# Kernel tuning notes

Measured on AMD Instinct MI355X. Metric: run time of the kernel, lower is better.

The kernel has to match this reference:

```python
import jax, jax.numpy as jnp
import numpy as np

B, T, D, H = 4, 2048, 1024, 16
DH = D // H  # 64


def setup_inputs() -> dict:
    key = jax.random.key(0)
    ks = jax.random.split(key, 6)
    s = 0.02
    x = jax.random.normal(ks[0], (B, T, D), dtype=jnp.float32)
    # causal mask: True (1) marks positions to be masked out
    mask = jnp.triu(jnp.ones((T, T), dtype=bool), k=1)[None, None, :, :]
    WQ = jax.random.normal(ks[1], (D, D), dtype=jnp.float32) * s
    WK = jax.random.normal(ks[2], (D, D), dtype=jnp.float32) * s
    WV = jax.random.normal(ks[3], (D, D), dtype=jnp.float32) * s
    WO = jax.random.normal(ks[4], (D, D), dtype=jnp.float32) * s
    z = jnp.zeros((D,), dtype=jnp.float32)
    return {"x": x, "mask": mask, "WQ": WQ, "bQ": z, "WK": WK, "bK": z,
            "WV": WV, "bV": z, "WO": WO, "bO": z}


def reference(x, mask, WQ, bQ, WK, bK, WV, bV, WO, bO):
    Bc, Tc, Dc = x.shape
    def split_heads(t):  # [B,T,D] -> [B,H,T,DH]
        return t.reshape(Bc, Tc, H, DH).transpose(0, 2, 1, 3)
    q = split_heads(x @ WQ + bQ)
    k = split_heads(x @ WK + bK)
    v = split_heads(x @ WV + bV)
    qk = jnp.einsum("bhqd,bhkd->bhqk", q, k) / jnp.sqrt(jnp.float32(DH))
    qk = qk + mask.astype(qk.dtype) * (-1e9)
    attn = jax.nn.softmax(qk, axis=-1)
    ctx = jnp.einsum("bhqk,bhkd->bhqd", attn, v)  # [B,H,T,DH]
    ctx = ctx.transpose(0, 2, 1, 3).reshape(Bc, Tc, Dc)
    return ctx @ WO + bO
```

## Files before the change

### kernel.cpp

```cpp
#include <hip/hip_runtime.h>
#include <hip/hip_bf16.h>
#include <stdint.h>

#define T_SEQ   2048
#define D_MODEL 1024
#define NHEAD   16
#define DHEAD   64
#define BATCH   4
#define MTOK    (BATCH * T_SEQ)

typedef __attribute__((ext_vector_type(4))) float f32x4;
typedef __attribute__((ext_vector_type(16))) float f32x16;
typedef __attribute__((ext_vector_type(8))) short bf16x8;
typedef __attribute__((ext_vector_type(4))) short s16x4;
typedef __attribute__((ext_vector_type(4))) unsigned u32x4;

__device__ __forceinline__ f32x4 mfma16(bf16x8 a, bf16x8 b, f32x4 c) {
  return __builtin_amdgcn_mfma_f32_16x16x32_bf16(a, b, c, 0, 0, 0);
}
__device__ __forceinline__ f32x16 mfma32(bf16x8 a, bf16x8 b, f32x16 c) {
  return __builtin_amdgcn_mfma_f32_32x32x16_bf16(a, b, c, 0, 0, 0);
}

__device__ __forceinline__ short f2bf(float f) {
  __hip_bfloat16 h = __float2bfloat16(f);
  return *reinterpret_cast<short*>(&h);
}

__device__ __forceinline__ unsigned cvtpk(float a, float b) {
  unsigned r;
  asm("v_cvt_pk_bf16_f32 %0, %1, %2" : "=v"(r) : "v"(a), "v"(b));
  return r;
}

union PB { u32x4 u; bf16x8 b; };

#define GLD_LDS16(gp, lp)                                                      \
  __builtin_amdgcn_global_load_lds(                                            \
      (const __attribute__((address_space(1))) void*)(gp),                     \
      (__attribute__((address_space(3))) void*)(lp), 16, 0, 0)

__global__ __launch_bounds__(256) void transpose_w_kernel(
    const float* __restrict__ W0, const float* __restrict__ W1,
    const float* __restrict__ W2, const float* __restrict__ W3,
    short* __restrict__ out)
{
  const int z = blockIdx.z;
  const float* W = (z == 0) ? W0 : (z == 1) ? W1 : (z == 2) ? W2 : W3;
  short* o = out + (size_t)z * D_MODEL * D_MODEL;
  __shared__ float tile[32][33];
  const int n0 = blockIdx.x * 32, k0 = blockIdx.y * 32;
  const int c = threadIdx.x & 31, r = threadIdx.x >> 5;
#pragma unroll
  for (int i = 0; i < 4; i++)
    tile[r + i * 8][c] = W[(size_t)(k0 + r + i * 8) * D_MODEL + n0 + c];
  __syncthreads();
#pragma unroll
  for (int i = 0; i < 4; i++)
    o[(size_t)(n0 + r + i * 8) * D_MODEL + k0 + c] = f2bf(tile[c][r + i * 8]);
}

__global__ __launch_bounds__(256) void cvt_x_kernel(
    const float* __restrict__ x, short* __restrict__ xb)
{
  const size_t i = (size_t)blockIdx.x * 256 + threadIdx.x;
  const float4 a = ((const float4*)x)[i * 2];
  const float4 b = ((const float4*)x)[i * 2 + 1];
  bf16x8 o;
  o[0] = f2bf(a.x); o[1] = f2bf(a.y); o[2] = f2bf(a.z); o[3] = f2bf(a.w);
  o[4] = f2bf(b.x); o[5] = f2bf(b.y); o[6] = f2bf(b.z); o[7] = f2bf(b.w);
  ((bf16x8*)xb)[i] = o;
}

__global__ __launch_bounds__(256) void gemm_bt(
    const short* __restrict__ A, const short* __restrict__ Bt,
    const float* __restrict__ bias, float* __restrict__ Cp)
{
  __shared__ __align__(16) short As[128 * 32];
  __shared__ __align__(16) short Bs[128 * 32];
  const int tid = threadIdx.x, lane = tid & 63, wid = tid >> 6;
  const int wr = wid >> 1, wc = wid & 1;
  const int lg = lane >> 4, ln = lane & 15;
  const int m0 = blockIdx.x * 128, n0 = blockIdx.y * 128;
  const int lrow = lane >> 2, lchunk = lane & 3;

  f32x4 acc[4][4];
#pragma unroll
  for (int i = 0; i < 4; i++)
#pragma unroll
    for (int j = 0; j < 4; j++) acc[i][j] = {0.f, 0.f, 0.f, 0.f};

  for (int k0 = 0; k0 < 1024; k0 += 32) {
#pragma unroll
    for (int s = 0; s < 2; ++s) {
      const int rbase = (wid * 2 + s) * 16;
      const short* gpa = A + (size_t)(m0 + rbase + lrow) * 1024 + k0 + lchunk * 8;
      GLD_LDS16(gpa, As + rbase * 32);
      const short* gpb = Bt + (size_t)(n0 + rbase + lrow) * 1024 + k0 + lchunk * 8;
      GLD_LDS16(gpb, Bs + rbase * 32);
    }
    __syncthreads();
    bf16x8 a[4], b[4];
#pragma unroll
    for (int mi = 0; mi < 4; mi++)
      a[mi] = *(const bf16x8*)(As + (wr * 64 + mi * 16 + ln) * 32 + lg * 8);
#pragma unroll
    for (int ni = 0; ni < 4; ni++)
      b[ni] = *(const bf16x8*)(Bs + (wc * 64 + ni * 16 + ln) * 32 + lg * 8);
#pragma unroll
    for (int mi = 0; mi < 4; mi++)
#pragma unroll
      for (int ni = 0; ni < 4; ni++)
        acc[mi][ni] = mfma16(a[mi], b[ni], acc[mi][ni]);
    __syncthreads();
  }

#pragma unroll
  for (int mi = 0; mi < 4; mi++)
#pragma unroll
    for (int ni = 0; ni < 4; ni++)
#pragma unroll
      for (int r = 0; r < 4; r++) {
        const int row = m0 + wr * 64 + mi * 16 + lg * 4 + r;
        const int col = n0 + wc * 64 + ni * 16 + ln;
        Cp[(size_t)row * 1024 + col] = acc[mi][ni][r] + bias[col];
      }
}

__global__ __launch_bounds__(256) void gemm_qkv(
    const short* __restrict__ A, const short* __restrict__ Wt,
    const float* __restrict__ bQ, const float* __restrict__ bK,
    const float* __restrict__ bV,
    short* __restrict__ Qb, short* __restrict__ Kb, short* __restrict__ Vb,
    float qscale)
{
  __shared__ __align__(16) short As[128 * 32];
  __shared__ __align__(16) short Bs[128 * 32];
  const int tid = threadIdx.x, lane = tid & 63, wid = tid >> 6;
  const int wr = wid >> 1, wc = wid & 1;
  const int lg = lane >> 4, ln = lane & 15;
  const int m0 = blockIdx.x * 128;
  const int nglob = blockIdx.y * 128;
  const int seg = blockIdx.y >> 3;
  const int n0 = nglob & 1023;
  const short* Bt = Wt + (size_t)nglob * 1024;
  const float* bias = (seg == 0) ? bQ : (seg == 1) ? bK : bV;
  short* Cp = (seg == 0) ? Qb : (seg == 1) ? Kb : Vb;
  const float scale = (seg == 0) ? qscale : 1.0f;
  const int lrow = lane >> 2, lchunk = lane & 3;

  f32x4 acc[4][4];
#pragma unroll
  for (int i = 0; i < 4; i++)
#pragma unroll
    for (int j = 0; j < 4; j++) acc[i][j] = {0.f, 0.f, 0.f, 0.f};

  for (int k0 = 0; k0 < 1024; k0 += 32) {
#pragma unroll
    for (int s = 0; s < 2; ++s) {
      const int rbase = (wid * 2 + s) * 16;
      const short* gpa = A + (size_t)(m0 + rbase + lrow) * 1024 + k0 + lchunk * 8;
      GLD_LDS16(gpa, As + rbase * 32);
      const short* gpb = Bt + (size_t)(rbase + lrow) * 1024 + k0 + lchunk * 8;
      GLD_LDS16(gpb, Bs + rbase * 32);
    }
    __syncthreads();
    bf16x8 a[4], b[4];
#pragma unroll
    for (int mi = 0; mi < 4; mi++)
      a[mi] = *(const bf16x8*)(As + (wr * 64 + mi * 16 + ln) * 32 + lg * 8);
#pragma unroll
    for (int ni = 0; ni < 4; ni++)
      b[ni] = *(const bf16x8*)(Bs + (wc * 64 + ni * 16 + ln) * 32 + lg * 8);
#pragma unroll
    for (int mi = 0; mi < 4; mi++)
#pragma unroll
      for (int ni = 0; ni < 4; ni++)
        acc[mi][ni] = mfma16(a[mi], b[ni], acc[mi][ni]);
    __syncthreads();
  }

#pragma unroll
  for (int mi = 0; mi < 4; mi++)
#pragma unroll
    for (int ni = 0; ni < 4; ni++)
#pragma unroll
      for (int r = 0; r < 4; r++) {
        const int row = m0 + wr * 64 + mi * 16 + lg * 4 + r;
        const int col = n0 + wc * 64 + ni * 16 + ln;
        const float v = (acc[mi][ni][r] + bias[col]) * scale;
        Cp[(size_t)row * 1024 + col] = f2bf(v);
      }
}

__global__ __launch_bounds__(256) void transpose_v_kernel(
    const short* __restrict__ V, short* __restrict__ Vt)
{
  const int bh = blockIdx.y, t0 = blockIdx.x * 64;
  const int b = bh >> 4, h = bh & 15;
  __shared__ __align__(16) short tile[64][72];
  const int tl = threadIdx.x >> 3, c = threadIdx.x & 7;
#pragma unroll
  for (int half = 0; half < 2; half++) {
    const int t = tl + half * 32;
    bf16x8 v = *(const bf16x8*)(V + (size_t)(b * T_SEQ + t0 + t) * 1024 + h * 64 + c * 8);
    *(bf16x8*)&tile[t][c * 8] = v;
  }
  __syncthreads();
#pragma unroll
  for (int half = 0; half < 2; half++) {
    const int dh = tl + half * 32;
    bf16x8 v;
#pragma unroll
    for (int j = 0; j < 8; j++) v[j] = tile[c * 8 + j][dh];
    *(bf16x8*)(Vt + ((size_t)bh * 64 + dh) * T_SEQ + t0 + c * 8) = v;
  }
}

__device__ __forceinline__ void tile_chain(
    const bf16x8* kf0, const bf16x8* kf1,
    const bf16x8* vf0, const bf16x8* vf1,
    const bf16x8* qf,
    f32x16& o0, f32x16& o1, float& m_run, float& l_run,
    const int kv0, const int qw, const int q, const int hi)
{
  f32x16 s0, s1;
#pragma unroll
  for (int i = 0; i < 16; i++) { s0[i] = 0.f; s1[i] = 0.f; }
  __builtin_amdgcn_s_setprio(1);
#pragma unroll
  for (int c = 0; c < 4; c++) s0 = mfma32(kf0[c], qf[c], s0);
#pragma unroll
  for (int c = 0; c < 4; c++) s1 = mfma32(kf1[c], qf[c], s1);
  __builtin_amdgcn_s_setprio(0);

  if (kv0 + 63 > qw) {
    const int qrel = q - kv0 - 4 * hi;
#pragma unroll
    for (int r = 0; r < 16; r++) {
      const int cst = (r & 3) + 8 * (r >> 2);
      if (cst > qrel) s0[r] = -3.0e38f;
      if (cst + 32 > qrel) s1[r] = -3.0e38f;
    }
  }

  float mx;
  {
    float t[8];
#pragma unroll
    for (int i = 0; i < 8; i++)
      t[i] = fmaxf(fmaxf(s0[i], s0[i + 8]), fmaxf(s1[i], s1[i + 8]));
    const float a0 = fmaxf(fmaxf(t[0], t[1]), fmaxf(t[2], t[3]));
    const float a1 = fmaxf(fmaxf(t[4], t[5]), fmaxf(t[6], t[7]));
    mx = fmaxf(a0, a1);
    mx = fmaxf(mx, __shfl_xor(mx, 32));
  }
  const float mn = fmaxf(m_run, mx);
  const float rr = exp2f(m_run - mn);
  m_run = mn;
#pragma unroll
  for (int i = 0; i < 16; i++) s0[i] = exp2f(s0[i] - mn);
#pragma unroll
  for (int i = 0; i < 16; i++) s1[i] = exp2f(s1[i] - mn);
  float ts;
  {
    float t[8];
#pragma unroll
    for (int i = 0; i < 8; i++) t[i] = (s0[i] + s0[i + 8]) + (s1[i] + s1[i + 8]);
    ts = ((t[0] + t[1]) + (t[2] + t[3])) + ((t[4] + t[5]) + (t[6] + t[7]));
    ts += __shfl_xor(ts, 32);
  }
  l_run = l_run * rr + ts;
#pragma unroll
  for (int i = 0; i < 16; i++) { o0[i] *= rr; o1[i] *= rr; }

  const bool low = (hi == 0);
  PB pb[4];
  {
    unsigned c0 = cvtpk(s0[0], s0[1]),   c1 = cvtpk(s0[2], s0[3]);
    unsigned c2 = cvtpk(s0[4], s0[5]),   c3 = cvtpk(s0[6], s0[7]);
    unsigned c4 = cvtpk(s0[8], s0[9]),   c5 = cvtpk(s0[10], s0[11]);
    unsigned c6 = cvtpk(s0[12], s0[13]), c7 = cvtpk(s0[14], s0[15]);
    unsigned d0 = __shfl_xor((int)c0, 32), d1 = __shfl_xor((int)c1, 32);
    unsigned d2 = __shfl_xor((int)c2, 32), d3 = __shfl_xor((int)c3, 32);
    unsigned d4 = __shfl_xor((int)c4, 32), d5 = __shfl_xor((int)c5, 32);
    unsigned d6 = __shfl_xor((int)c6, 32), d7 = __shfl_xor((int)c7, 32);
    pb[0].u = (u32x4){low ? c0 : d2, low ? c1 : d3, low ? d0 : c2, low ? d1 : c3};
    pb[1].u = (u32x4){low ? c4 : d6, low ? c5 : d7, low ? d4 : c6, low ? d5 : c7};
  }
  {
    unsigned c0 = cvtpk(s1[0], s1[1]),   c1 = cvtpk(s1[2], s1[3]);
    unsigned c2 = cvtpk(s1[4], s1[5]),   c3 = cvtpk(s1[6], s1[7]);
    unsigned c4 = cvtpk(s1[8], s1[9]),   c5 = cvtpk(s1[10], s1[11]);
    unsigned c6 = cvtpk(s1[12], s1[13]), c7 = cvtpk(s1[14], s1[15]);
    unsigned d0 = __shfl_xor((int)c0, 32), d1 = __shfl_xor((int)c1, 32);
    unsigned d2 = __shfl_xor((int)c2, 32), d3 = __shfl_xor((int)c3, 32);
    unsigned d4 = __shfl_xor((int)c4, 32), d5 = __shfl_xor((int)c5, 32);
    unsigned d6 = __shfl_xor((int)c6, 32), d7 = __shfl_xor((int)c7, 32);
    pb[2].u = (u32x4){low ? c0 : d2, low ? c1 : d3, low ? d0 : c2, low ? d1 : c3};
    pb[3].u = (u32x4){low ? c4 : d6, low ? c5 : d7, low ? d4 : c6, low ? d5 : c7};
  }

  __builtin_amdgcn_s_setprio(1);
#pragma unroll
  for (int kc = 0; kc < 4; kc++) {
    o0 = mfma32(vf0[kc], pb[kc].b, o0);
    o1 = mfma32(vf1[kc], pb[kc].b, o1);
  }
  __builtin_amdgcn_s_setprio(0);
}

__device__ __forceinline__ void attn_epilogue(
    short* cp, const f32x16& o0, const f32x16& o1, float l_run, int hi)
{
  const float inv = 1.0f / l_run;
#pragma unroll
  for (int g = 0; g < 4; g++) {
    s16x4 w0, w1;
#pragma unroll
    for (int j = 0; j < 4; j++) {
      w0[j] = f2bf(o0[g * 4 + j] * inv);
      w1[j] = f2bf(o1[g * 4 + j] * inv);
    }
    *(s16x4*)(cp + g * 8 + 4 * hi) = w0;
    *(s16x4*)(cp + 32 + g * 8 + 4 * hi) = w1;
  }
}

#define LOADK(dst0, dst1, itv)                                                 \
  {                                                                            \
    const short* kp = K + (size_t)(b * T_SEQ + (itv) * 64 + lq) * 1024 +       \
                      h * 64 + hi * 8;                                         \
    _Pragma("unroll")                                                          \
    for (int c = 0; c < 4; c++) {                                              \
      dst0[c] = *(const bf16x8*)(kp + c * 16);                                 \
      dst1[c] = *(const bf16x8*)(kp + 32 * 1024 + c * 16);                     \
    }                                                                          \
  }

#define LOADV(dst0, dst1, itv)                                                 \
  {                                                                            \
    const short* vp = Vt + (size_t)(bh * 64 + lq) * T_SEQ + (itv) * 64 +       \
                      hi * 8;                                                  \
    _Pragma("unroll")                                                          \
    for (int c = 0; c < 4; c++) {                                              \
      dst0[c] = *(const bf16x8*)(vp + c * 16);                                 \
      dst1[c] = *(const bf16x8*)(vp + 32 * T_SEQ + c * 16);                    \
    }                                                                          \
  }

__global__ __launch_bounds__(256, 2) void attn_fwd(
    const short* __restrict__ Q, const short* __restrict__ K,
    const short* __restrict__ Vt, short* __restrict__ ctx)
{
  const int tid = threadIdx.x, lane = tid & 63, wid = tid >> 6;
  const int hi = lane >> 5, lq = lane & 31;
  const int id = (int)blockIdx.x;
  const int bh = (id & 7) * 8 + ((id >> 3) & 7);
  const int p = (id >> 6) * 4 + wid;
  const int b = bh >> 4, h = bh & 15;

  const int qtA = p, qtB = 63 - p;
  const int qwA = qtA * 32, qwB = qtB * 32;
  const int qA = qwA + lq, qB = qwB + lq;

  bf16x8 qfA[4], qfB[4];
  {
    const short* qpA = Q + (size_t)(b * T_SEQ + qA) * 1024 + h * 64 + hi * 8;
    const short* qpB = Q + (size_t)(b * T_SEQ + qB) * 1024 + h * 64 + hi * 8;
#pragma unroll
    for (int c = 0; c < 4; c++) {
      qfA[c] = *(const bf16x8*)(qpA + c * 16);
      qfB[c] = *(const bf16x8*)(qpB + c * 16);
    }
  }

  f32x16 oA0, oA1, oB0, oB1;
#pragma unroll
  for (int i = 0; i < 16; i++) { oA0[i] = 0.f; oA1[i] = 0.f; oB0[i] = 0.f; oB1[i] = 0.f; }
  float mA = -3.0e38f, lA = 0.f, mB = -3.0e38f, lB = 0.f;

  const int ntA = (qwA + 95) >> 6, ntB = (qwB + 95) >> 6;

  bf16x8 kP0[4], kP1[4], kQ0[4], kQ1[4];
  LOADK(kP0, kP1, 0);

  int it = 0;
#pragma unroll 1
  for (; it + 2 <= ntB; it += 2) {
    {
      bf16x8 vf0[4], vf1[4];
      LOADV(vf0, vf1, it);
      LOADK(kQ0, kQ1, it + 1);
      tile_chain(kP0, kP1, vf0, vf1, qfB, oB0, oB1, mB, lB, it * 64, qwB, qB, hi);
      if (it < ntA)
        tile_chain(kP0, kP1, vf0, vf1, qfA, oA0, oA1, mA, lA, it * 64, qwA, qA, hi);
    }
    {
      bf16x8 vf0[4], vf1[4];
      LOADV(vf0, vf1, it + 1);
      if (it + 2 < ntB) LOADK(kP0, kP1, it + 2);
      tile_chain(kQ0, kQ1, vf0, vf1, qfB, oB0, oB1, mB, lB, (it + 1) * 64, qwB, qB, hi);
      if (it + 1 < ntA)
        tile_chain(kQ0, kQ1, vf0, vf1, qfA, oA0, oA1, mA, lA, (it + 1) * 64, qwA, qA, hi);
    }
  }
  if (it < ntB) {
    bf16x8 vf0[4], vf1[4];
    LOADV(vf0, vf1, it);
    tile_chain(kP0, kP1, vf0, vf1, qfB, oB0, oB1, mB, lB, it * 64, qwB, qB, hi);
    if (it < ntA)
      tile_chain(kP0, kP1, vf0, vf1, qfA, oA0, oA1, mA, lA, it * 64, qwA, qA, hi);
  }

  attn_epilogue(ctx + (size_t)(b * T_SEQ + qA) * 1024 + h * 64, oA0, oA1, lA, hi);
  attn_epilogue(ctx + (size_t)(b * T_SEQ + qB) * 1024 + h * 64, oB0, oB1, lB, hi);
}

extern "C" void kernel_launch(void* const* d_in, const int* in_sizes, int n_in,
                              void* d_out, int out_size, void* d_ws, size_t ws_size,
                              hipStream_t stream)
{
  (void)in_sizes; (void)n_in; (void)out_size; (void)ws_size;
  const float* x  = (const float*)d_in[0];
  const float* WQ = (const float*)d_in[2];
  const float* bQ = (const float*)d_in[3];
  const float* WK = (const float*)d_in[4];
  const float* bK = (const float*)d_in[5];
  const float* WV = (const float*)d_in[6];
  const float* bV = (const float*)d_in[7];
  const float* WO = (const float*)d_in[8];
  const float* bO = (const float*)d_in[9];
  float* out = (float*)d_out;

  const size_t MB = 1024ull * 1024ull;
  char* w = (char*)d_ws;
  short* xb = (short*)(w);
  short* Wt = (short*)(w + 16 * MB);
  short* Qb = (short*)(w + 24 * MB);
  short* Kb = (short*)(w + 40 * MB);
  short* Vb = (short*)(w + 56 * MB);
  short* Vt = (short*)(w + 72 * MB);
  short* ctx = xb;

  transpose_w_kernel<<<dim3(32, 32, 4), 256, 0, stream>>>(WQ, WK, WV, WO, Wt);
  cvt_x_kernel<<<dim3(MTOK * D_MODEL / 8 / 256), 256, 0, stream>>>(x, xb);

  const float qscale = 0.125f * 1.4426950408889634f;
  gemm_qkv<<<dim3(64, 24), 256, 0, stream>>>(xb, Wt, bQ, bK, bV, Qb, Kb, Vb, qscale);

  transpose_v_kernel<<<dim3(32, 64), 256, 0, stream>>>(Vb, Vt);
  attn_fwd<<<dim3(512), 256, 0, stream>>>(Qb, Kb, Vt, ctx);

  gemm_bt<<<dim3(64, 8), 256, 0, stream>>>(ctx, Wt + 3ull * D_MODEL * D_MODEL, bO, out);
}
```

Before: 220.7 us.

## Rewrite attention with 16x16 MFMA tiles, sequential pair passes, higher occupancy

The attention kernel moves from 32x32x16 MFMA tiles, where each wave holds two 32-row query tiles and double-buffered K fragments, to 16x16x32 MFMA with 16-row query tiles handled one after another in two passes. Register use drops, so launch bounds rise to four blocks per SM and the grid doubles to 1024 blocks. The aim is better latency hiding and load balance through occupancy. In exchange it drops K prefetching and the sharing of K/V loads across the two query tiles, adds more cross-lane shuffles to relayout P, and gets less data reuse per load.

New measurement: 344.3 us. 56.0% more time.

```diff
diff --git a/kernel.cpp b/kernel.cpp
--- a/kernel.cpp
+++ b/kernel.cpp
@@ -10,16 +10,12 @@
 #define MTOK    (BATCH * T_SEQ)
 
 typedef __attribute__((ext_vector_type(4))) float f32x4;
-typedef __attribute__((ext_vector_type(16))) float f32x16;
 typedef __attribute__((ext_vector_type(8))) short bf16x8;
 typedef __attribute__((ext_vector_type(4))) short s16x4;
 typedef __attribute__((ext_vector_type(4))) unsigned u32x4;
 
 __device__ __forceinline__ f32x4 mfma16(bf16x8 a, bf16x8 b, f32x4 c) {
   return __builtin_amdgcn_mfma_f32_16x16x32_bf16(a, b, c, 0, 0, 0);
-}
-__device__ __forceinline__ f32x16 mfma32(bf16x8 a, bf16x8 b, f32x16 c) {
-  return __builtin_amdgcn_mfma_f32_32x32x16_bf16(a, b, c, 0, 0, 0);
 }
 
 __device__ __forceinline__ short f2bf(float f) {
@@ -217,204 +213,143 @@
   }
 }
 
-__device__ __forceinline__ void tile_chain(
-    const bf16x8* kf0, const bf16x8* kf1,
-    const bf16x8* vf0, const bf16x8* vf1,
-    const bf16x8* qf,
-    f32x16& o0, f32x16& o1, float& m_run, float& l_run,
-    const int kv0, const int qw, const int q, const int hi)
-{
-  f32x16 s0, s1;
-#pragma unroll
-  for (int i = 0; i < 16; i++) { s0[i] = 0.f; s1[i] = 0.f; }
-  __builtin_amdgcn_s_setprio(1);
-#pragma unroll
-  for (int c = 0; c < 4; c++) s0 = mfma32(kf0[c], qf[c], s0);
-#pragma unroll
-  for (int c = 0; c < 4; c++) s1 = mfma32(kf1[c], qf[c], s1);
-  __builtin_amdgcn_s_setprio(0);
-
-  if (kv0 + 63 > qw) {
-    const int qrel = q - kv0 - 4 * hi;
-#pragma unroll
-    for (int r = 0; r < 16; r++) {
-      const int cst = (r & 3) + 8 * (r >> 2);
-      if (cst > qrel) s0[r] = -3.0e38f;
-      if (cst + 32 > qrel) s1[r] = -3.0e38f;
-    }
-  }
-
-  float mx;
-  {
-    float t[8];
-#pragma unroll
-    for (int i = 0; i < 8; i++)
-      t[i] = fmaxf(fmaxf(s0[i], s0[i + 8]), fmaxf(s1[i], s1[i + 8]));
-    const float a0 = fmaxf(fmaxf(t[0], t[1]), fmaxf(t[2], t[3]));
-    const float a1 = fmaxf(fmaxf(t[4], t[5]), fmaxf(t[6], t[7]));
-    mx = fmaxf(a0, a1);
-    mx = fmaxf(mx, __shfl_xor(mx, 32));
-  }
-  const float mn = fmaxf(m_run, mx);
-  const float rr = exp2f(m_run - mn);
-  m_run = mn;
-#pragma unroll
-  for (int i = 0; i < 16; i++) s0[i] = exp2f(s0[i] - mn);
-#pragma unroll
-  for (int i = 0; i < 16; i++) s1[i] = exp2f(s1[i] - mn);
-  float ts;
-  {
-    float t[8];
-#pragma unroll
-    for (int i = 0; i < 8; i++) t[i] = (s0[i] + s0[i + 8]) + (s1[i] + s1[i + 8]);
-    ts = ((t[0] + t[1]) + (t[2] + t[3])) + ((t[4] + t[5]) + (t[6] + t[7]));
-    ts += __shfl_xor(ts, 32);
-  }
-  l_run = l_run * rr + ts;
-#pragma unroll
-  for (int i = 0; i < 16; i++) { o0[i] *= rr; o1[i] *= rr; }
-
-  const bool low = (hi == 0);
-  PB pb[4];
-  {
-    unsigned c0 = cvtpk(s0[0], s0[1]),   c1 = cvtpk(s0[2], s0[3]);
-    unsigned c2 = cvtpk(s0[4], s0[5]),   c3 = cvtpk(s0[6], s0[7]);
-    unsigned c4 = cvtpk(s0[8], s0[9]),   c5 = cvtpk(s0[10], s0[11]);
-    unsigned c6 = cvtpk(s0[12], s0[13]), c7 = cvtpk(s0[14], s0[15]);
-    unsigned d0 = __shfl_xor((int)c0, 32), d1 = __shfl_xor((int)c1, 32);
-    unsigned d2 = __shfl_xor((int)c2, 32), d3 = __shfl_xor((int)c3, 32);
-    unsigned d4 = __shfl_xor((int)c4, 32), d5 = __shfl_xor((int)c5, 32);
-    unsigned d6 = __shfl_xor((int)c6, 32), d7 = __shfl_xor((int)c7, 32);
-    pb[0].u = (u32x4){low ? c0 : d2, low ? c1 : d3, low ? d0 : c2, low ? d1 : c3};
-    pb[1].u = (u32x4){low ? c4 : d6, low ? c5 : d7, low ? d4 : c6, low ? d5 : c7};
-  }
-  {
-    unsigned c0 = cvtpk(s1[0], s1[1]),   c1 = cvtpk(s1[2], s1[3]);
-    unsigned c2 = cvtpk(s1[4], s1[5]),   c3 = cvtpk(s1[6], s1[7]);
-    unsigned c4 = cvtpk(s1[8], s1[9]),   c5 = cvtpk(s1[10], s1[11]);
-    unsigned c6 = cvtpk(s1[12], s1[13]), c7 = cvtpk(s1[14], s1[15]);
-    unsigned d0 = __shfl_xor((int)c0, 32), d1 = __shfl_xor((int)c1, 32);
-    unsigned d2 = __shfl_xor((int)c2, 32), d3 = __shfl_xor((int)c3, 32);
-    unsigned d4 = __shfl_xor((int)c4, 32), d5 = __shfl_xor((int)c5, 32);
-    unsigned d6 = __shfl_xor((int)c6, 32), d7 = __shfl_xor((int)c7, 32);
-    pb[2].u = (u32x4){low ? c0 : d2, low ? c1 : d3, low ? d0 : c2, low ? d1 : c3};
-    pb[3].u = (u32x4){low ? c4 : d6, low ? c5 : d7, low ? d4 : c6, low ? d5 : c7};
-  }
-
-  __builtin_amdgcn_s_setprio(1);
-#pragma unroll
-  for (int kc = 0; kc < 4; kc++) {
-    o0 = mfma32(vf0[kc], pb[kc].b, o0);
-    o1 = mfma32(vf1[kc], pb[kc].b, o1);
-  }
-  __builtin_amdgcn_s_setprio(0);
-}
-
-__device__ __forceinline__ void attn_epilogue(
-    short* cp, const f32x16& o0, const f32x16& o1, float l_run, int hi)
-{
-  const float inv = 1.0f / l_run;
-#pragma unroll
-  for (int g = 0; g < 4; g++) {
-    s16x4 w0, w1;
-#pragma unroll
-    for (int j = 0; j < 4; j++) {
-      w0[j] = f2bf(o0[g * 4 + j] * inv);
-      w1[j] = f2bf(o1[g * 4 + j] * inv);
-    }
-    *(s16x4*)(cp + g * 8 + 4 * hi) = w0;
-    *(s16x4*)(cp + 32 + g * 8 + 4 * hi) = w1;
-  }
-}
-
-#define LOADK(dst0, dst1, itv)                                                 \
-  {                                                                            \
-    const short* kp = K + (size_t)(b * T_SEQ + (itv) * 64 + lq) * 1024 +       \
-                      h * 64 + hi * 8;                                         \
-    _Pragma("unroll")                                                          \
-    for (int c = 0; c < 4; c++) {                                              \
-      dst0[c] = *(const bf16x8*)(kp + c * 16);                                 \
-      dst1[c] = *(const bf16x8*)(kp + 32 * 1024 + c * 16);                     \
-    }                                                                          \
-  }
-
-#define LOADV(dst0, dst1, itv)                                                 \
-  {                                                                            \
-    const short* vp = Vt + (size_t)(bh * 64 + lq) * T_SEQ + (itv) * 64 +       \
-                      hi * 8;                                                  \
-    _Pragma("unroll")                                                          \
-    for (int c = 0; c < 4; c++) {                                              \
-      dst0[c] = *(const bf16x8*)(vp + c * 16);                                 \
-      dst1[c] = *(const bf16x8*)(vp + 32 * T_SEQ + c * 16);                    \
-    }                                                                          \
-  }
-
-__global__ __launch_bounds__(256, 2) void attn_fwd(
+__global__ __launch_bounds__(256, 4) void attn_fwd(
     const short* __restrict__ Q, const short* __restrict__ K,
     const short* __restrict__ Vt, short* __restrict__ ctx)
 {
   const int tid = threadIdx.x, lane = tid & 63, wid = tid >> 6;
-  const int hi = lane >> 5, lq = lane & 31;
+  const int ln = lane & 15, lg = lane >> 4;
   const int id = (int)blockIdx.x;
   const int bh = (id & 7) * 8 + ((id >> 3) & 7);
   const int p = (id >> 6) * 4 + wid;
   const int b = bh >> 4, h = bh & 15;
 
-  const int qtA = p, qtB = 63 - p;
-  const int qwA = qtA * 32, qwB = qtB * 32;
-  const int qA = qwA + lq, qB = qwB + lq;
-
-  bf16x8 qfA[4], qfB[4];
-  {
-    const short* qpA = Q + (size_t)(b * T_SEQ + qA) * 1024 + h * 64 + hi * 8;
-    const short* qpB = Q + (size_t)(b * T_SEQ + qB) * 1024 + h * 64 + hi * 8;
-#pragma unroll
-    for (int c = 0; c < 4; c++) {
-      qfA[c] = *(const bf16x8*)(qpA + c * 16);
-      qfB[c] = *(const bf16x8*)(qpB + c * 16);
-    }
-  }
-
-  f32x16 oA0, oA1, oB0, oB1;
-#pragma unroll
-  for (int i = 0; i < 16; i++) { oA0[i] = 0.f; oA1[i] = 0.f; oB0[i] = 0.f; oB1[i] = 0.f; }
-  float mA = -3.0e38f, lA = 0.f, mB = -3.0e38f, lB = 0.f;
-
-  const int ntA = (qwA + 95) >> 6, ntB = (qwB + 95) >> 6;
-
-  bf16x8 kP0[4], kP1[4], kQ0[4], kQ1[4];
-  LOADK(kP0, kP1, 0);
-
-  int it = 0;
 #pragma unroll 1
-  for (; it + 2 <= ntB; it += 2) {
+  for (int pass = 0; pass < 2; ++pass) {
+    const int qt = pass ? (127 - p) : p;
+    const int qw = qt * 16;
+    const int q = qw + ln;
+
+    bf16x8 qf0, qf1;
     {
-      bf16x8 vf0[4], vf1[4];
-      LOADV(vf0, vf1, it);
-      LOADK(kQ0, kQ1, it + 1);
-      tile_chain(kP0, kP1, vf0, vf1, qfB, oB0, oB1, mB, lB, it * 64, qwB, qB, hi);
-      if (it < ntA)
-        tile_chain(kP0, kP1, vf0, vf1, qfA, oA0, oA1, mA, lA, it * 64, qwA, qA, hi);
-    }
-    {
-      bf16x8 vf0[4], vf1[4];
-      LOADV(vf0, vf1, it + 1);
-      if (it + 2 < ntB) LOADK(kP0, kP1, it + 2);
-      tile_chain(kQ0, kQ1, vf0, vf1, qfB, oB0, oB1, mB, lB, (it + 1) * 64, qwB, qB, hi);
-      if (it + 1 < ntA)
-        tile_chain(kQ0, kQ1, vf0, vf1, qfA, oA0, oA1, mA, lA, (it + 1) * 64, qwA, qA, hi);
-    }
-  }
-  if (it < ntB) {
-    bf16x8 vf0[4], vf1[4];
-    LOADV(vf0, vf1, it);
-    tile_chain(kP0, kP1, vf0, vf1, qfB, oB0, oB1, mB, lB, it * 64, qwB, qB, hi);
-    if (it < ntA)
-      tile_chain(kP0, kP1, vf0, vf1, qfA, oA0, oA1, mA, lA, it * 64, qwA, qA, hi);
-  }
-
-  attn_epilogue(ctx + (size_t)(b * T_SEQ + qA) * 1024 + h * 64, oA0, oA1, lA, hi);
-  attn_epilogue(ctx + (size_t)(b * T_SEQ + qB) * 1024 + h * 64, oB0, oB1, lB, hi);
+      const short* qp = Q + (size_t)(b * T_SEQ + q) * 1024 + h * 64 + lg * 8;
+      qf0 = *(const bf16x8*)qp;
+      qf1 = *(const bf16x8*)(qp + 32);
+    }
+
+    f32x4 o[4];
+#pragma unroll
+    for (int i = 0; i < 4; i++) o[i] = {0.f, 0.f, 0.f, 0.f};
+    float m_run = -3.0e38f, l_run = 0.f;
+
+    const int nt = (qw + 79) >> 6;
+#pragma unroll 1
+    for (int it = 0; it < nt; ++it) {
+      const int kv0 = it * 64;
+      bf16x8 kf[4][2];
+      {
+        const short* kp = K + (size_t)(b * T_SEQ + kv0 + ln) * 1024 + h * 64 + lg * 8;
+#pragma unroll
+        for (int g = 0; g < 4; g++) {
+          kf[g][0] = *(const bf16x8*)(kp + g * 16 * 1024);
+          kf[g][1] = *(const bf16x8*)(kp + g * 16 * 1024 + 32);
+        }
+      }
+      f32x4 s[4];
+      __builtin_amdgcn_s_setprio(1);
+#pragma unroll
+      for (int g = 0; g < 4; g++) {
+        f32x4 z = {0.f, 0.f, 0.f, 0.f};
+        z = mfma16(kf[g][0], qf0, z);
+        s[g] = mfma16(kf[g][1], qf1, z);
+      }
+      __builtin_amdgcn_s_setprio(0);
+      bf16x8 vt[4][2];
+      {
+        const short* vp = Vt + (size_t)(bh * 64 + ln) * T_SEQ + kv0 + lg * 8;
+#pragma unroll
+        for (int d = 0; d < 4; d++) {
+          vt[d][0] = *(const bf16x8*)(vp + d * 16 * T_SEQ);
+          vt[d][1] = *(const bf16x8*)(vp + d * 16 * T_SEQ + 32);
+        }
+      }
+      if (kv0 + 63 > qw) {
+        const int qrel = q - kv0 - lg * 4;
+#pragma unroll
+        for (int g = 0; g < 4; g++)
+#pragma unroll
+          for (int r = 0; r < 4; r++)
+            if (g * 16 + r > qrel) s[g][r] = -3.0e38f;
+      }
+      float mx;
+      {
+        float t0 = fmaxf(fmaxf(s[0][0], s[0][1]), fmaxf(s[0][2], s[0][3]));
+        float t1 = fmaxf(fmaxf(s[1][0], s[1][1]), fmaxf(s[1][2], s[1][3]));
+        float t2 = fmaxf(fmaxf(s[2][0], s[2][1]), fmaxf(s[2][2], s[2][3]));
+        float t3 = fmaxf(fmaxf(s[3][0], s[3][1]), fmaxf(s[3][2], s[3][3]));
+        mx = fmaxf(fmaxf(t0, t1), fmaxf(t2, t3));
+        mx = fmaxf(mx, __shfl_xor(mx, 16));
+        mx = fmaxf(mx, __shfl_xor(mx, 32));
+      }
+      const float mn = fmaxf(m_run, mx);
+      const float rr = exp2f(m_run - mn);
+      m_run = mn;
+#pragma unroll
+      for (int g = 0; g < 4; g++)
+#pragma unroll
+        for (int r = 0; r < 4; r++) s[g][r] = exp2f(s[g][r] - mn);
+      float ts;
+      {
+        float t0 = (s[0][0] + s[0][1]) + (s[0][2] + s[0][3]);
+        float t1 = (s[1][0] + s[1][1]) + (s[1][2] + s[1][3]);
+        float t2 = (s[2][0] + s[2][1]) + (s[2][2] + s[2][3]);
+        float t3 = (s[3][0] + s[3][1]) + (s[3][2] + s[3][3]);
+        ts = (t0 + t1) + (t2 + t3);
+        ts += __shfl_xor(ts, 16);
+        ts += __shfl_xor(ts, 32);
+      }
+      l_run = l_run * rr + ts;
+#pragma unroll
+      for (int i = 0; i < 4; i++) o[i] *= rr;
+
+      const unsigned u00 = cvtpk(s[0][0], s[0][1]), u01 = cvtpk(s[0][2], s[0][3]);
+      const unsigned u10 = cvtpk(s[1][0], s[1][1]), u11 = cvtpk(s[1][2], s[1][3]);
+      const unsigned u20 = cvtpk(s[2][0], s[2][1]), u21 = cvtpk(s[2][2], s[2][3]);
+      const unsigned u30 = cvtpk(s[3][0], s[3][1]), u31 = cvtpk(s[3][2], s[3][3]);
+      const int srcA = ln + ((lg & 1) * 2) * 16;
+      const int srcB = srcA + 16;
+      const bool gl = (lg < 2);
+      PB p0, p1;
+      {
+        unsigned a, c;
+        a = __shfl((int)u00, srcA); c = __shfl((int)u10, srcA); p0.u[0] = gl ? a : c;
+        a = __shfl((int)u01, srcA); c = __shfl((int)u11, srcA); p0.u[1] = gl ? a : c;
+        a = __shfl((int)u00, srcB); c = __shfl((int)u10, srcB); p0.u[2] = gl ? a : c;
+        a = __shfl((int)u01, srcB); c = __shfl((int)u11, srcB); p0.u[3] = gl ? a : c;
+        a = __shfl((int)u20, srcA); c = __shfl((int)u30, srcA); p1.u[0] = gl ? a : c;
+        a = __shfl((int)u21, srcA); c = __shfl((int)u31, srcA); p1.u[1] = gl ? a : c;
+        a = __shfl((int)u20, srcB); c = __shfl((int)u30, srcB); p1.u[2] = gl ? a : c;
+        a = __shfl((int)u21, srcB); c = __shfl((int)u31, srcB); p1.u[3] = gl ? a : c;
+      }
+      __builtin_amdgcn_s_setprio(1);
+#pragma unroll
+      for (int d = 0; d < 4; d++) {
+        o[d] = mfma16(vt[d][0], p0.b, o[d]);
+        o[d] = mfma16(vt[d][1], p1.b, o[d]);
+      }
+      __builtin_amdgcn_s_setprio(0);
+    }
+
+    const float inv = 1.0f / l_run;
+    short* cp = ctx + (size_t)(b * T_SEQ + q) * 1024 + h * 64 + lg * 4;
+#pragma unroll
+    for (int d = 0; d < 4; d++) {
+      s16x4 w;
+#pragma unroll
+      for (int r = 0; r < 4; r++) w[r] = f2bf(o[d][r] * inv);
+      *(s16x4*)(cp + d * 16) = w;
+    }
+  }
 }
 
 extern "C" void kernel_launch(void* const* d_in, const int* in_sizes, int n_in,
@@ -450,7 +385,7 @@
   gemm_qkv<<<dim3(64, 24), 256, 0, stream>>>(xb, Wt, bQ, bK, bV, Qb, Kb, Vb, qscale);
 
   transpose_v_kernel<<<dim3(32, 64), 256, 0, stream>>>(Vb, Vt);
-  attn_fwd<<<dim3(512), 256, 0, stream>>>(Qb, Kb, Vt, ctx);
+  attn_fwd<<<dim3(1024), 256, 0, stream>>>(Qb, Kb, Vt, ctx);
 
   gemm_bt<<<dim3(64, 8), 256, 0, stream>>>(ctx, Wt + 3ull * D_MODEL * D_MODEL, bO, out);
 }
```
